# Kernel tuning notes

Measured on AMD Instinct MI355X. Metric: run time of the kernel, lower is better.

The kernel has to match this reference:

```python
import jax, jax.numpy as jnp
import numpy as np

C = 1.0        # curvature parameter (manifold curvature -1/C)
EPS = 1e-7


def expmap0_space(v, k):
    # v: [..., ds] spatial tangent vector at the hyperboloid origin (time comp 0)
    # returns ambient point [..., ds+1] = (sqrt(k)cosh(|v|/sqrt(k)), sqrt(k)sinh(|v|/sqrt(k)) v/|v|)
    sk = jnp.sqrt(k)
    n = jnp.maximum(jnp.linalg.norm(v, axis=-1, keepdims=True), EPS)
    t = sk * jnp.cosh(n / sk)
    s = sk * jnp.sinh(n / sk) * (v / n)
    return jnp.concatenate([t, s], axis=-1)


def logmap0_space(p, k):
    # p: [..., ds+1] hyperboloid point -> spatial tangent [..., ds] at origin
    sk = jnp.sqrt(k)
    t, s = p[..., :1], p[..., 1:]
    ns = jnp.maximum(jnp.linalg.norm(s, axis=-1, keepdims=True), EPS)
    d = sk * jnp.arccosh(jnp.maximum(t / sk, 1.0 + EPS))
    return d * (s / ns)


def setup_inputs() -> dict:
    key = jax.random.key(0)
    N, DS, E = 50000, 127, 800000
    ks = jax.random.split(key, 8)
    x = jax.random.normal(ks[0], (N, DS), dtype=jnp.float32) * 0.1
    edge_src = jax.random.randint(ks[1], (E,), 0, N)
    edge_dst = jax.random.randint(ks[2], (E,), 0, N)
    edge_weight = jax.random.uniform(ks[3], (E,), dtype=jnp.float32) / 16.0  # ~1/deg norm
    sc = 1.0 / np.sqrt(DS)
    W1 = jax.random.normal(ks[4], (DS, DS), dtype=jnp.float32) * sc
    b1 = jnp.zeros((DS,), dtype=jnp.float32)
    W2 = jax.random.normal(ks[5], (DS, DS), dtype=jnp.float32) * sc
    b2 = jnp.zeros((DS,), dtype=jnp.float32)
    return {"x": x, "W1": W1, "b1": b1, "W2": W2, "b2": b2,
            "edge_src": edge_src, "edge_dst": edge_dst, "edge_weight": edge_weight}


def reference(x, W1, b1, W2, b2, edge_src, edge_dst, edge_weight):
    N = x.shape[0]
    # encode(): cat zero time column + expmap0 onto hyperboloid
    p = expmap0_space(x, C)                 # [N, ds+1]
    h = logmap0_space(p, C)                 # tangent features at origin [N, ds]
    for (W, b) in ((W1, b1), (W2, b2)):
        # hyperbolic linear in tangent space
        z = h @ W + b                       # [N, ds]
        # adjacency-based neighbor aggregation (sparse spmm via edge list)
        msg = edge_weight[:, None] * z[edge_src]          # [E, ds] irregular gather
        agg = jax.ops.segment_sum(msg, edge_dst, num_segments=N)
        # activation + skip connection, back onto the manifold between layers
        h = jax.nn.relu(agg) + h
        h = logmap0_space(expmap0_space(h, C), C)
    return expmap0_space(h, C)              # [N, ds+1] on hyperboloid
```

## Files before the change

kernel.cpp:

```cpp
#include <hip/hip_runtime.h>

#define EPS 1e-7f
#define DS 127
#define DP 128
#define NBMAX 512
#define CAP 4096
#define CH 2048
#define PADB ((DP * DP + DP + 255) / 256)
#define BM 64

typedef short bf16x8 __attribute__((ext_vector_type(8)));
typedef float f32x4  __attribute__((ext_vector_type(4)));
typedef float f32x2  __attribute__((ext_vector_type(2)));

__device__ __forceinline__ float wave_sum(float v) {
#pragma unroll
    for (int off = 32; off > 0; off >>= 1)
        v += __shfl_xor(v, off, 64);
    return v;
}

__device__ __forceinline__ int wave_sum_i(int v) {
#pragma unroll
    for (int off = 32; off > 0; off >>= 1)
        v += __shfl_xor(v, off, 64);
    return v;
}

__device__ __forceinline__ unsigned short f2bf(float f) {
    unsigned u = __float_as_uint(f);
    unsigned r = (u + 0x7FFFu + ((u >> 16) & 1u)) >> 16;
    return (unsigned short)r;
}

__device__ __forceinline__ unsigned pack_bf2(float a, float b) {
    return (unsigned)f2bf(a) | ((unsigned)f2bf(b) << 16);
}

__device__ __forceinline__ unsigned char f2fp8(float v) {
    return (unsigned char)(__builtin_amdgcn_cvt_pk_fp8_f32(v, v, 0, false) & 0xFF);
}

__device__ __forceinline__ float logexp_scale(float n2) {
    float nrm = sqrtf(n2);
    return (nrm >= 4.472136e-4f) ? 1.0f : (4.472136e-4f / fmaxf(nrm, EPS));
}

__device__ __forceinline__ void sinhcosh(float n, float& sh, float& ch) {
    float e  = __expf(n);
    float em = __expf(-n);
    sh = 0.5f * (e - em);
    ch = 0.5f * (e + em);
}

__device__ __forceinline__ void padT_dev(int pb, int tid,
        const float* __restrict__ W, const float* __restrict__ b,
        unsigned short* __restrict__ Wt, float* __restrict__ bp) {
    int i = pb * 256 + tid;
    if (i < DP * DP) {
        int n = i >> 7, k = i & (DP - 1);
        Wt[i] = (k < DS && n < DS) ? f2bf(W[k * DS + n]) : (unsigned short)0;
    } else if (i < DP * DP + DP) {
        int j = i - DP * DP;
        bp[j] = (j < DS) ? b[j] : 0.f;
    }
}

__device__ void binA_dev(int abid, int tid,
        const int* __restrict__ es, const int* __restrict__ ed,
        const float* __restrict__ ew,
        int* __restrict__ gcnt, unsigned* __restrict__ stg_pk,
        unsigned char* __restrict__ stg_r, int E) {
    __shared__ int  lcnt[NBMAX];
    __shared__ int  loff[NBMAX];
    __shared__ int  gbase[NBMAX];
    __shared__ unsigned       lst_pk[CH];
    __shared__ unsigned short lst_d[CH];

    int lane = tid & 63;
    int base = abid * CH;
    int cnt  = min(CH, E - base);

    for (int b = tid; b < NBMAX; b += 256) lcnt[b] = 0;
    __syncthreads();

    unsigned pk[CH / 256];
    int      rd[CH / 256];
#pragma unroll
    for (int k = 0; k < CH / 256; k++) {
        int i = base + k * 256 + tid;
        if (i < E) {
            int d = ed[i];
            rd[k] = d;
            pk[k] = ((unsigned)f2bf(ew[i]) << 16) | (unsigned)es[i];
            atomicAdd(&lcnt[d >> 7], 1);
        } else {
            rd[k] = -1;
        }
    }
    __syncthreads();

    if (tid < 64) {
        int carry = 0;
        for (int c = 0; c < NBMAX; c += 64) {
            int v = lcnt[c + lane];
            int inc = v;
#pragma unroll
            for (int off = 1; off < 64; off <<= 1) {
                int t = __shfl_up(inc, off, 64);
                if (lane >= off) inc += t;
            }
            loff[c + lane] = carry + inc - v;
            carry += __shfl(inc, 63, 64);
        }
    }
    __syncthreads();
    for (int b = tid; b < NBMAX; b += 256) lcnt[b] = 0;
    __syncthreads();

#pragma unroll
    for (int k = 0; k < CH / 256; k++) {
        if (rd[k] >= 0) {
            int b = rd[k] >> 7;
            int slot = loff[b] + atomicAdd(&lcnt[b], 1);
            lst_pk[slot] = pk[k];
            lst_d[slot]  = (unsigned short)rd[k];
        }
    }
    __syncthreads();

    for (int b = tid; b < NBMAX; b += 256) {
        int c = lcnt[b];
        gbase[b] = c ? atomicAdd(&gcnt[b], c) : 0;
    }
    __syncthreads();

    for (int s = tid; s < cnt; s += 256) {
        unsigned p = lst_pk[s];
        int d = lst_d[s];
        int b = d >> 7;
        int idx = gbase[b] + (s - loff[b]);
        if (idx >= CAP) idx = CAP - 1;
        stg_pk[(size_t)b * CAP + idx] = p;
        stg_r [(size_t)b * CAP + idx] = (unsigned char)(d & 127);
    }
}

__device__ void binB_dev(int b, int tid,
        const unsigned* __restrict__ stg_pk, const unsigned char* __restrict__ stg_r,
        const int* __restrict__ gcnt,
        int* __restrict__ row_start, unsigned* __restrict__ epk,
        int N, int E) {
    __shared__ int rcnt[128];
    __shared__ int roff[128];
    __shared__ int sh_bb;

    int lane = tid & 63;
    int wave = tid >> 6;
    int cnt  = min(gcnt[b], CAP);
    const unsigned*      in_pk = stg_pk + (size_t)b * CAP;
    const unsigned char* in_r  = stg_r  + (size_t)b * CAP;

    if (tid < 128) rcnt[tid] = 0;
    if (b == 0 && tid == 0) row_start[N] = E;
    __syncthreads();

    if (wave == 3) {
        int acc = 0;
        for (int c = lane; c < b; c += 64) acc += min(gcnt[c], CAP);
        acc = wave_sum_i(acc);
        if (lane == 0) sh_bb = acc;
    } else {
        int n4 = cnt >> 2;
        const uchar4* in_r4 = (const uchar4*)in_r;
        for (int i = tid; i < n4; i += 192) {
            uchar4 v = in_r4[i];
            atomicAdd(&rcnt[v.x], 1);
            atomicAdd(&rcnt[v.y], 1);
            atomicAdd(&rcnt[v.z], 1);
            atomicAdd(&rcnt[v.w], 1);
        }
        for (int i = (n4 << 2) + tid; i < cnt; i += 192)
            atomicAdd(&rcnt[in_r[i]], 1);
    }
    __syncthreads();
    int bb = sh_bb;

    if (tid < 64) {
        int carry = 0;
        for (int c = 0; c < 128; c += 64) {
            int v = rcnt[c + lane];
            int inc = v;
#pragma unroll
            for (int off = 1; off < 64; off <<= 1) {
                int t = __shfl_up(inc, off, 64);
                if (lane >= off) inc += t;
            }
            roff[c + lane] = carry + inc - v;
            carry += __shfl(inc, 63, 64);
        }
    }
    __syncthreads();

    if (tid < 128) {
        int row = b * 128 + tid;
        if (row < N) row_start[row] = bb + roff[tid];
        rcnt[tid] = 0;
    }
    __syncthreads();

    for (int i = tid; i < cnt; i += 256) {
        int r = in_r[i];
        int pos = atomicAdd(&rcnt[r], 1);
        epk[bb + roff[r] + pos] = in_pk[i];
    }
}

__global__ __launch_bounds__(256) void k1_kernel(
        const int* __restrict__ es, const int* __restrict__ ed,
        const float* __restrict__ ew,
        int* __restrict__ gcnt, unsigned* __restrict__ stg_pk,
        unsigned char* __restrict__ stg_r, int E,
        const float* __restrict__ W1, const float* __restrict__ b1,
        unsigned short* __restrict__ Wt1, float* __restrict__ bp1,
        const float* __restrict__ W2, const float* __restrict__ b2,
        unsigned short* __restrict__ Wt2, float* __restrict__ bp2, int nA) {
    int bid = blockIdx.x;
    int tid = threadIdx.x;
    if (bid < nA) {
        binA_dev(bid, tid, es, ed, ew, gcnt, stg_pk, stg_r, E);
        return;
    }
    bid -= nA;
    int layer = (bid >= PADB);
    int pb    = bid - layer * PADB;
    padT_dev(pb, tid, layer ? W2 : W1, layer ? b2 : b1,
             layer ? Wt2 : Wt1, layer ? bp2 : bp1);
}

__device__ void fgemm_dev(int gbid, int tid,
        const float* __restrict__ x, unsigned* __restrict__ hbu,
        const unsigned short* __restrict__ Wt, const float* __restrict__ bp,
        unsigned char* __restrict__ z8, int N) {
    __shared__ unsigned sha[64 * 64];

    int wave = tid >> 6;
    int lane = tid & 63;
    int r0   = gbid * BM;

    f32x2 xv[16];
#pragma unroll
    for (int r = 0; r < 16; r++) {
        int row = r0 + wave * 16 + r;
        if (row < N) {
            const float* rp = x + (size_t)row * DS;
            xv[r].x = rp[2 * lane];
            xv[r].y = (lane < 63) ? rp[2 * lane + 1] : 0.f;
        } else {
            xv[r].x = 0.f; xv[r].y = 0.f;
        }
    }
#pragma unroll
    for (int r = 0; r < 16; r++) {
        int lr  = wave * 16 + r;
        int row = r0 + lr;
        float s = logexp_scale(wave_sum(xv[r].x * xv[r].x + xv[r].y * xv[r].y));
        unsigned pk = pack_bf2(s * xv[r].x, (lane < 63) ? s * xv[r].y : 0.f);
        sha[lr * 64 + lane] = pk;
        if (row < N) hbu[(size_t)row * (DP / 2) + lane] = pk;
    }

    int m    = lane & 15;
    int quad = lane >> 4;

    f32x4 acc[8];
#pragma unroll
    for (int t = 0; t < 8; t++) acc[t] = (f32x4){0.f, 0.f, 0.f, 0.f};

    const unsigned* shrow = sha + (size_t)(wave * 16 + m) * 64;
    bf16x8 a[4];
#pragma unroll
    for (int kq = 0; kq < 4; kq++)
        a[kq] = *(const bf16x8*)(shrow + kq * 16 + quad * 4);

#pragma unroll
    for (int kq = 0; kq < 4; kq++) {
#pragma unroll
        for (int nt = 0; nt < 8; nt++) {
            bf16x8 bfr = ((const bf16x8*)(Wt + (size_t)(nt * 16 + m) * DP))[kq * 4 + quad];
            acc[nt] = __builtin_amdgcn_mfma_f32_16x16x32_bf16(a[kq], bfr, acc[nt], 0, 0, 0);
        }
    }

    int rw0 = r0 + wave * 16;
#pragma unroll
    for (int nt = 0; nt < 8; nt++) {
        float bias = bp[nt * 16 + m];
#pragma unroll
        for (int reg = 0; reg < 4; reg++) {
            int row = rw0 + quad * 4 + reg;
            if (row < N)
                z8[(size_t)row * DP + nt * 16 + m] = f2fp8(acc[nt][reg] + bias);
        }
    }
}

__global__ __launch_bounds__(256) void k2_kernel(
        const unsigned* __restrict__ stg_pk, const unsigned char* __restrict__ stg_r,
        const int* __restrict__ gcnt,
        int* __restrict__ row_start, unsigned* __restrict__ epk,
        const float* __restrict__ x, unsigned* __restrict__ hbu,
        const unsigned short* __restrict__ Wt, const float* __restrict__ bp,
        unsigned char* __restrict__ z8, int N, int E, int nB) {
    int bid = blockIdx.x;
    int tid = threadIdx.x;
    if (bid < nB) {
        binB_dev(bid, tid, stg_pk, stg_r, gcnt, row_start, epk, N, E);
        return;
    }
    fgemm_dev(bid - nB, tid, x, hbu, Wt, bp, z8, N);
}

__global__ __launch_bounds__(256) void gemm_kernel(
        const unsigned short* __restrict__ hb,
        const unsigned short* __restrict__ Wt,
        const float* __restrict__ bp,
        unsigned char* __restrict__ z8, int N) {
    int wave = threadIdx.x >> 6;
    int lane = threadIdx.x & 63;
    int m    = lane & 15;
    int quad = lane >> 4;
    int r0   = blockIdx.x * BM + wave * 16;

    f32x4 acc[8];
#pragma unroll
    for (int t = 0; t < 8; t++) acc[t] = (f32x4){0.f, 0.f, 0.f, 0.f};

    const bf16x8* arow = (const bf16x8*)(hb + (size_t)(r0 + m) * DP);
    bf16x8 a[4];
#pragma unroll
    for (int kq = 0; kq < 4; kq++) a[kq] = arow[kq * 4 + quad];

#pragma unroll
    for (int kq = 0; kq < 4; kq++) {
#pragma unroll
        for (int nt = 0; nt < 8; nt++) {
            bf16x8 bfr = ((const bf16x8*)(Wt + (size_t)(nt * 16 + m) * DP))[kq * 4 + quad];
            acc[nt] = __builtin_amdgcn_mfma_f32_16x16x32_bf16(a[kq], bfr, acc[nt], 0, 0, 0);
        }
    }

#pragma unroll
    for (int nt = 0; nt < 8; nt++) {
        float bias = bp[nt * 16 + m];
#pragma unroll
        for (int reg = 0; reg < 4; reg++) {
            int row = r0 + quad * 4 + reg;
            if (row < N)
                z8[(size_t)row * DP + nt * 16 + m] = f2fp8(acc[nt][reg] + bias);
        }
    }
}

__device__ __forceinline__ void gather16(const unsigned char* __restrict__ zc,
        const unsigned* __restrict__ epk, int e, int lane2,
        float& a0, float& a1) {
    unsigned pks[16], us[16];
#pragma unroll
    for (int i = 0; i < 16; i++) pks[i] = epk[e + i];
#pragma unroll
    for (int i = 0; i < 16; i++)
        us[i] = *(const unsigned short*)(zc + (((pks[i] & 0xFFFFu) << 7) + lane2));
#pragma unroll
    for (int i = 0; i < 16; i++) {
        float wf = __uint_as_float(pks[i] & 0xFFFF0000u);
        f32x2 zv = __builtin_amdgcn_cvt_pk_f32_fp8(us[i], false);
        a0 = fmaf(wf, zv.x, a0);
        a1 = fmaf(wf, zv.y, a1);
    }
}

__device__ __forceinline__ void gather_tail16(const unsigned char* __restrict__ zc,
        const unsigned* __restrict__ epk, int e, int end, int lane2,
        float& a0, float& a1) {
    unsigned pks[16], us[16];
#pragma unroll
    for (int i = 0; i < 16; i++) {
        int ii = e + i;
        int ic = (ii < end) ? ii : (end - 1);
        unsigned p = epk[ic];
        pks[i] = (ii < end) ? p : 0u;
    }
#pragma unroll
    for (int i = 0; i < 16; i++)
        us[i] = *(const unsigned short*)(zc + (((pks[i] & 0xFFFFu) << 7) + lane2));
#pragma unroll
    for (int i = 0; i < 16; i++) {
        float wf = __uint_as_float(pks[i] & 0xFFFF0000u);
        f32x2 zv = __builtin_amdgcn_cvt_pk_f32_fp8(us[i], false);
        a0 = fmaf(wf, zv.x, a0);
        a1 = fmaf(wf, zv.y, a1);
    }
}

template <bool LAST>
__global__ __launch_bounds__(256) void agg_f_tpl(
                          const unsigned char* __restrict__ zc,
                          const unsigned* __restrict__ hbu_in,
                          const int* __restrict__ row_start,
                          const unsigned* __restrict__ epk,
                          unsigned* __restrict__ hbu_out,
                          float* __restrict__ out, int N) {
    int wid  = (int)((blockIdx.x * blockDim.x + threadIdx.x) >> 6);
    int lane = threadIdx.x & 63;
    int gw0  = wid * 2;
    if (gw0 >= N) return;
    gw0 = __builtin_amdgcn_readfirstlane(gw0);
    int lane2 = lane << 1;
    bool has1 = (gw0 + 1 < N);

    int rs0 = row_start[gw0];
    int rs1 = row_start[gw0 + 1];
    int rs2 = has1 ? row_start[gw0 + 2] : rs1;
    unsigned hu0 = hbu_in[(size_t)gw0 * (DP / 2) + lane];
    unsigned hu1 = has1 ? hbu_in[(size_t)(gw0 + 1) * (DP / 2) + lane] : 0u;

    int begs[2] = {rs0, rs1};
    int ends[2] = {rs1, rs2};
    float a0[2] = {0.f, 0.f}, a1[2] = {0.f, 0.f};

#pragma unroll
    for (int r = 0; r < 2; r++) {
        int e = begs[r], end = ends[r];
        for (; e + 16 <= end; e += 16) gather16(zc, epk, e, lane2, a0[r], a1[r]);
        if (e < end) gather_tail16(zc, epk, e, end, lane2, a0[r], a1[r]);
    }

    unsigned hus[2] = {hu0, hu1};
#pragma unroll
    for (int r = 0; r < 2; r++) {
        if (r == 1 && !has1) break;
        int gw = gw0 + r;
        float x0 = __uint_as_float(hus[r] << 16) + fmaxf(a0[r], 0.f);
        float x1 = (lane < 63) ? __uint_as_float(hus[r] & 0xFFFF0000u) + fmaxf(a1[r], 0.f)
                               : 0.f;

        float n2 = wave_sum(x0 * x0 + x1 * x1);
        float scale = logexp_scale(n2);
        float y0 = scale * x0;
        float y1 = (lane < 63) ? scale * x1 : 0.f;

        if (!LAST) {
            hbu_out[(size_t)gw * (DP / 2) + lane] = pack_bf2(y0, y1);
        } else {
            float n2y = scale * scale * n2;
            float ny  = fmaxf(sqrtf(n2y), EPS);
            float shy, chy;
            sinhcosh(ny, shy, chy);
            float sc  = shy / ny;
            float* orow = out + (size_t)gw * DP;
            if (lane == 0) orow[0] = chy;
            orow[1 + 2 * lane] = sc * y0;
            if (lane < 63) orow[2 + 2 * lane] = sc * y1;
        }
    }
}

extern "C" void kernel_launch(void* const* d_in, const int* in_sizes, int n_in,
                              void* d_out, int out_size, void* d_ws, size_t ws_size,
                              hipStream_t stream) {
    const float* x  = (const float*)d_in[0];
    const float* W1 = (const float*)d_in[1];
    const float* b1 = (const float*)d_in[2];
    const float* W2 = (const float*)d_in[3];
    const float* b2 = (const float*)d_in[4];
    const int*   es = (const int*)d_in[5];
    const int*   ed = (const int*)d_in[6];
    const float* ew = (const float*)d_in[7];

    const int N  = in_sizes[0] / DS;
    const int E  = in_sizes[5];
    const int NR = (N + BM - 1) / BM * BM;
    const int NB = (N + 127) >> 7;

    unsigned short* hb  = (unsigned short*)d_ws;
    unsigned char*  z8  = (unsigned char*)(hb + (size_t)NR * DP);
    unsigned short* Wt1 = (unsigned short*)(z8 + (size_t)N * DP);
    unsigned short* Wt2 = Wt1 + DP * DP;
    float* bp1          = (float*)(Wt2 + DP * DP);
    float* bp2          = bp1 + DP;
    unsigned* epk       = (unsigned*)(bp2 + DP);
    int*   row_start    = (int*)(epk + E);
    int*   gcnt         = row_start + N + 1;
    unsigned* stg_pk    = (unsigned*)(gcnt + NBMAX);
    unsigned char* stg_r = (unsigned char*)(stg_pk + (size_t)NBMAX * CAP);

    unsigned* hbu = (unsigned*)hb;

    const int gemmBlocks = (N + BM - 1) / BM;
    const int binABlocks = (E + CH - 1) / CH;
    const int aggWaves   = (N + 1) / 2;
    const int aggBlocks  = (aggWaves + 3) / 4;

    hipMemsetAsync(gcnt, 0, NBMAX * sizeof(int), stream);

    k1_kernel<<<binABlocks + 2 * PADB, 256, 0, stream>>>(
        es, ed, ew, gcnt, stg_pk, stg_r, E,
        W1, b1, Wt1, bp1, W2, b2, Wt2, bp2, binABlocks);

    k2_kernel<<<NB + gemmBlocks, 256, 0, stream>>>(
        stg_pk, stg_r, gcnt, row_start, epk,
        x, hbu, Wt1, bp1, z8, N, E, NB);

    agg_f_tpl<false><<<aggBlocks, 256, 0, stream>>>(z8, hbu, row_start, epk,
                                                    hbu, nullptr, N);

    gemm_kernel<<<gemmBlocks, 256, 0, stream>>>(hb, Wt2, bp2, z8, N);

    agg_f_tpl<true><<<aggBlocks, 256, 0, stream>>>(z8, hbu, row_start, epk,
                                                   nullptr, (float*)d_out, N);
}
```

Baseline: 223.2 us.

## Fuse layer-1 aggregation with layer-2 GEMM via shared-memory staging

Merges the first aggregation kernel and the second-layer GEMM into one kernel. Each block aggregates its 64 rows, stages the bf16 results in LDS and runs the MFMA GEMM from there, writing fp8 z into a new second buffer (z8b) so other blocks' gathers from the old z are not overwritten. This removes a kernel launch and the global round trip of h before the GEMM. The cost is lower parallelism in the aggregation phase, since each wave handles 8 row pairs serially, plus LDS use and an extra N*128-byte workspace buffer.

```diff
diff --git a/kernel.cpp b/kernel.cpp
--- a/kernel.cpp
+++ b/kernel.cpp
@@ -321,47 +321,6 @@
     fgemm_dev(bid - nB, tid, x, hbu, Wt, bp, z8, N);
 }
 
-__global__ __launch_bounds__(256) void gemm_kernel(
-        const unsigned short* __restrict__ hb,
-        const unsigned short* __restrict__ Wt,
-        const float* __restrict__ bp,
-        unsigned char* __restrict__ z8, int N) {
-    int wave = threadIdx.x >> 6;
-    int lane = threadIdx.x & 63;
-    int m    = lane & 15;
-    int quad = lane >> 4;
-    int r0   = blockIdx.x * BM + wave * 16;
-
-    f32x4 acc[8];
-#pragma unroll
-    for (int t = 0; t < 8; t++) acc[t] = (f32x4){0.f, 0.f, 0.f, 0.f};
-
-    const bf16x8* arow = (const bf16x8*)(hb + (size_t)(r0 + m) * DP);
-    bf16x8 a[4];
-#pragma unroll
-    for (int kq = 0; kq < 4; kq++) a[kq] = arow[kq * 4 + quad];
-
-#pragma unroll
-    for (int kq = 0; kq < 4; kq++) {
-#pragma unroll
-        for (int nt = 0; nt < 8; nt++) {
-            bf16x8 bfr = ((const bf16x8*)(Wt + (size_t)(nt * 16 + m) * DP))[kq * 4 + quad];
-            acc[nt] = __builtin_amdgcn_mfma_f32_16x16x32_bf16(a[kq], bfr, acc[nt], 0, 0, 0);
-        }
-    }
-
-#pragma unroll
-    for (int nt = 0; nt < 8; nt++) {
-        float bias = bp[nt * 16 + m];
-#pragma unroll
-        for (int reg = 0; reg < 4; reg++) {
-            int row = r0 + quad * 4 + reg;
-            if (row < N)
-                z8[(size_t)row * DP + nt * 16 + m] = f2fp8(acc[nt][reg] + bias);
-        }
-    }
-}
-
 __device__ __forceinline__ void gather16(const unsigned char* __restrict__ zc,
         const unsigned* __restrict__ epk, int e, int lane2,
         float& a0, float& a1) {
@@ -403,14 +362,112 @@
     }
 }
 
-template <bool LAST>
-__global__ __launch_bounds__(256) void agg_f_tpl(
-                          const unsigned char* __restrict__ zc,
-                          const unsigned* __restrict__ hbu_in,
-                          const int* __restrict__ row_start,
-                          const unsigned* __restrict__ epk,
-                          unsigned* __restrict__ hbu_out,
-                          float* __restrict__ out, int N) {
+__device__ __forceinline__ void agg_pair(const unsigned char* __restrict__ zc,
+        const unsigned* __restrict__ hbu_in,
+        const int* __restrict__ row_start, const unsigned* __restrict__ epk,
+        int gw0, int lane, int lane2, int N,
+        unsigned py[2]) {
+    bool v0 = (gw0 < N);
+    bool v1 = (gw0 + 1 < N);
+    int rs0 = v0 ? row_start[gw0]     : 0;
+    int rs1 = v0 ? row_start[gw0 + 1] : 0;
+    int rs2 = v1 ? row_start[gw0 + 2] : rs1;
+    unsigned hu0 = v0 ? hbu_in[(size_t)gw0 * (DP / 2) + lane]       : 0u;
+    unsigned hu1 = v1 ? hbu_in[(size_t)(gw0 + 1) * (DP / 2) + lane] : 0u;
+
+    int begs[2] = {rs0, rs1};
+    int ends[2] = {rs1, rs2};
+    float a0[2] = {0.f, 0.f}, a1[2] = {0.f, 0.f};
+
+#pragma unroll
+    for (int r = 0; r < 2; r++) {
+        int e = begs[r], end = ends[r];
+        for (; e + 16 <= end; e += 16) gather16(zc, epk, e, lane2, a0[r], a1[r]);
+        if (e < end) gather_tail16(zc, epk, e, end, lane2, a0[r], a1[r]);
+    }
+
+    unsigned hus[2] = {hu0, hu1};
+#pragma unroll
+    for (int r = 0; r < 2; r++) {
+        float x0 = __uint_as_float(hus[r] << 16) + fmaxf(a0[r], 0.f);
+        float x1 = (lane < 63) ? __uint_as_float(hus[r] & 0xFFFF0000u) + fmaxf(a1[r], 0.f)
+                               : 0.f;
+        float n2 = wave_sum(x0 * x0 + x1 * x1);
+        float scale = logexp_scale(n2);
+        py[r] = pack_bf2(scale * x0, (lane < 63) ? scale * x1 : 0.f);
+    }
+}
+
+__global__ __launch_bounds__(256) void k3_kernel(
+        const unsigned char* __restrict__ zc,
+        unsigned* __restrict__ hbu,
+        const int* __restrict__ row_start,
+        const unsigned* __restrict__ epk,
+        const unsigned short* __restrict__ Wt,
+        const float* __restrict__ bp,
+        unsigned char* __restrict__ z8b,
+        int N) {
+    __shared__ unsigned sha[64 * 64];
+
+    int tid = threadIdx.x;
+    int w   = tid >> 6;
+    int ln  = tid & 63;
+    int ln2 = ln << 1;
+    int r0  = blockIdx.x * BM + w * 16;
+
+#pragma unroll 1
+    for (int p = 0; p < 8; p++) {
+        int gw0 = __builtin_amdgcn_readfirstlane(r0 + 2 * p);
+        unsigned py[2];
+        agg_pair(zc, hbu, row_start, epk, gw0, ln, ln2, N, py);
+        int lr = w * 16 + 2 * p;
+        sha[lr * 64 + ln]       = (gw0 < N)     ? py[0] : 0u;
+        sha[(lr + 1) * 64 + ln] = (gw0 + 1 < N) ? py[1] : 0u;
+        if (gw0 < N)     hbu[(size_t)gw0 * (DP / 2) + ln]       = py[0];
+        if (gw0 + 1 < N) hbu[(size_t)(gw0 + 1) * (DP / 2) + ln] = py[1];
+    }
+
+    int m    = ln & 15;
+    int quad = ln >> 4;
+
+    f32x4 acc[8];
+#pragma unroll
+    for (int t = 0; t < 8; t++) acc[t] = (f32x4){0.f, 0.f, 0.f, 0.f};
+
+    const unsigned* shrow = sha + (size_t)(w * 16 + m) * 64;
+    bf16x8 a[4];
+#pragma unroll
+    for (int kq = 0; kq < 4; kq++)
+        a[kq] = *(const bf16x8*)(shrow + kq * 16 + quad * 4);
+
+#pragma unroll
+    for (int kq = 0; kq < 4; kq++) {
+#pragma unroll
+        for (int nt = 0; nt < 8; nt++) {
+            bf16x8 bfr = ((const bf16x8*)(Wt + (size_t)(nt * 16 + m) * DP))[kq * 4 + quad];
+            acc[nt] = __builtin_amdgcn_mfma_f32_16x16x32_bf16(a[kq], bfr, acc[nt], 0, 0, 0);
+        }
+    }
+
+    int rw0 = blockIdx.x * BM + w * 16;
+#pragma unroll
+    for (int nt = 0; nt < 8; nt++) {
+        float bias = bp[nt * 16 + m];
+#pragma unroll
+        for (int reg = 0; reg < 4; reg++) {
+            int row = rw0 + quad * 4 + reg;
+            if (row < N)
+                z8b[(size_t)row * DP + nt * 16 + m] = f2fp8(acc[nt][reg] + bias);
+        }
+    }
+}
+
+__global__ __launch_bounds__(256) void k4_kernel(
+        const unsigned char* __restrict__ zc,
+        const unsigned* __restrict__ hbu_in,
+        const int* __restrict__ row_start,
+        const unsigned* __restrict__ epk,
+        float* __restrict__ out, int N) {
     int wid  = (int)((blockIdx.x * blockDim.x + threadIdx.x) >> 6);
     int lane = threadIdx.x & 63;
     int gw0  = wid * 2;
@@ -450,19 +507,15 @@
         float y0 = scale * x0;
         float y1 = (lane < 63) ? scale * x1 : 0.f;
 
-        if (!LAST) {
-            hbu_out[(size_t)gw * (DP / 2) + lane] = pack_bf2(y0, y1);
-        } else {
-            float n2y = scale * scale * n2;
-            float ny  = fmaxf(sqrtf(n2y), EPS);
-            float shy, chy;
-            sinhcosh(ny, shy, chy);
-            float sc  = shy / ny;
-            float* orow = out + (size_t)gw * DP;
-            if (lane == 0) orow[0] = chy;
-            orow[1 + 2 * lane] = sc * y0;
-            if (lane < 63) orow[2 + 2 * lane] = sc * y1;
-        }
+        float n2y = scale * scale * n2;
+        float ny  = fmaxf(sqrtf(n2y), EPS);
+        float shy, chy;
+        sinhcosh(ny, shy, chy);
+        float sc  = shy / ny;
+        float* orow = out + (size_t)gw * DP;
+        if (lane == 0) orow[0] = chy;
+        orow[1 + 2 * lane] = sc * y0;
+        if (lane < 63) orow[2 + 2 * lane] = sc * y1;
     }
 }
 
@@ -485,7 +538,8 @@
 
     unsigned short* hb  = (unsigned short*)d_ws;
     unsigned char*  z8  = (unsigned char*)(hb + (size_t)NR * DP);
-    unsigned short* Wt1 = (unsigned short*)(z8 + (size_t)N * DP);
+    unsigned char*  z8b = z8 + (size_t)N * DP;
+    unsigned short* Wt1 = (unsigned short*)(z8b + (size_t)N * DP);
     unsigned short* Wt2 = Wt1 + DP * DP;
     float* bp1          = (float*)(Wt2 + DP * DP);
     float* bp2          = bp1 + DP;
@@ -512,11 +566,9 @@
         stg_pk, stg_r, gcnt, row_start, epk,
         x, hbu, Wt1, bp1, z8, N, E, NB);
 
-    agg_f_tpl<false><<<aggBlocks, 256, 0, stream>>>(z8, hbu, row_start, epk,
-                                                    hbu, nullptr, N);
-
-    gemm_kernel<<<gemmBlocks, 256, 0, stream>>>(hb, Wt2, bp2, z8, N);
-
-    agg_f_tpl<true><<<aggBlocks, 256, 0, stream>>>(z8, hbu, row_start, epk,
-                                                   nullptr, (float*)d_out, N);
-}
+    k3_kernel<<<gemmBlocks, 256, 0, stream>>>(
+        z8, hbu, row_start, epk, Wt2, bp2, z8b, N);
+
+    k4_kernel<<<aggBlocks, 256, 0, stream>>>(
+        z8b, hbu, row_start, epk, (float*)d_out, N);
+}
```

Result: no change. 221.9 us (-0.6%).

## Split wave into half-waves gathering alternate edges with 4-byte fp8 loads

Applied to the files above, without the earlier changes.

The aggregation kernel now has each half-wave handle alternating edges. Each lane loads 4 fp8 features per edge as a single 32-bit load instead of 2 bytes, and the two half-wave partial sums are combined with a cross-half shuffle. Both rows' first 32-edge rounds are issued together to expose more independent memory requests. The intent is to halve the number of gather instructions per edge and raise memory-level parallelism. In exchange it reads edge entries past the row end, masked to weight zero, and uses more registers. The histogram loop also drops its uchar4 vectorisation in favour of a plain byte loop.

```diff
diff --git a/kernel.cpp b/kernel.cpp
--- a/kernel.cpp
+++ b/kernel.cpp
@@ -171,16 +171,7 @@
         acc = wave_sum_i(acc);
         if (lane == 0) sh_bb = acc;
     } else {
-        int n4 = cnt >> 2;
-        const uchar4* in_r4 = (const uchar4*)in_r;
-        for (int i = tid; i < n4; i += 192) {
-            uchar4 v = in_r4[i];
-            atomicAdd(&rcnt[v.x], 1);
-            atomicAdd(&rcnt[v.y], 1);
-            atomicAdd(&rcnt[v.z], 1);
-            atomicAdd(&rcnt[v.w], 1);
-        }
-        for (int i = (n4 << 2) + tid; i < cnt; i += 192)
+        for (int i = tid; i < cnt; i += 192)
             atomicAdd(&rcnt[in_r[i]], 1);
     }
     __syncthreads();
@@ -362,44 +353,81 @@
     }
 }
 
-__device__ __forceinline__ void gather16(const unsigned char* __restrict__ zc,
-        const unsigned* __restrict__ epk, int e, int lane2,
-        float& a0, float& a1) {
-    unsigned pks[16], us[16];
-#pragma unroll
-    for (int i = 0; i < 16; i++) pks[i] = epk[e + i];
-#pragma unroll
-    for (int i = 0; i < 16; i++)
-        us[i] = *(const unsigned short*)(zc + (((pks[i] & 0xFFFFu) << 7) + lane2));
+__device__ __forceinline__ void agg_round32(
+        const unsigned char* __restrict__ zc, const unsigned* __restrict__ epk,
+        int e, int end, bool lo, int q4, float* A) {
+    unsigned p[32];
+#pragma unroll
+    for (int i = 0; i < 32; i++) {
+        unsigned v = epk[e + i];
+        p[i] = (e + i < end) ? v : 0u;
+    }
+    unsigned ud[16];
 #pragma unroll
     for (int i = 0; i < 16; i++) {
-        float wf = __uint_as_float(pks[i] & 0xFFFF0000u);
-        f32x2 zv = __builtin_amdgcn_cvt_pk_f32_fp8(us[i], false);
-        a0 = fmaf(wf, zv.x, a0);
-        a1 = fmaf(wf, zv.y, a1);
-    }
-}
-
-__device__ __forceinline__ void gather_tail16(const unsigned char* __restrict__ zc,
-        const unsigned* __restrict__ epk, int e, int end, int lane2,
-        float& a0, float& a1) {
-    unsigned pks[16], us[16];
+        unsigned sel = lo ? p[2 * i] : p[2 * i + 1];
+        ud[i] = *(const unsigned*)(zc + (((size_t)(sel & 0xFFFFu)) << 7) + q4);
+    }
 #pragma unroll
     for (int i = 0; i < 16; i++) {
-        int ii = e + i;
-        int ic = (ii < end) ? ii : (end - 1);
-        unsigned p = epk[ic];
-        pks[i] = (ii < end) ? p : 0u;
-    }
-#pragma unroll
-    for (int i = 0; i < 16; i++)
-        us[i] = *(const unsigned short*)(zc + (((pks[i] & 0xFFFFu) << 7) + lane2));
+        unsigned sel = lo ? p[2 * i] : p[2 * i + 1];
+        float wf = __uint_as_float(sel & 0xFFFF0000u);
+        f32x2 zl = __builtin_amdgcn_cvt_pk_f32_fp8(ud[i], false);
+        f32x2 zh = __builtin_amdgcn_cvt_pk_f32_fp8(ud[i], true);
+        A[0] = fmaf(wf, zl.x, A[0]);
+        A[1] = fmaf(wf, zl.y, A[1]);
+        A[2] = fmaf(wf, zh.x, A[2]);
+        A[3] = fmaf(wf, zh.y, A[3]);
+    }
+}
+
+__device__ __forceinline__ void agg_round32_pair(
+        const unsigned char* __restrict__ zc, const unsigned* __restrict__ epk,
+        int e0, int end0, int e1, int end1, bool lo, int q4,
+        float* A, float* B) {
+    unsigned p0[32], p1[32];
+#pragma unroll
+    for (int i = 0; i < 32; i++) {
+        unsigned v = epk[e0 + i];
+        p0[i] = (e0 + i < end0) ? v : 0u;
+    }
+#pragma unroll
+    for (int i = 0; i < 32; i++) {
+        unsigned v = epk[e1 + i];
+        p1[i] = (e1 + i < end1) ? v : 0u;
+    }
+    unsigned ud0[16], ud1[16];
 #pragma unroll
     for (int i = 0; i < 16; i++) {
-        float wf = __uint_as_float(pks[i] & 0xFFFF0000u);
-        f32x2 zv = __builtin_amdgcn_cvt_pk_f32_fp8(us[i], false);
-        a0 = fmaf(wf, zv.x, a0);
-        a1 = fmaf(wf, zv.y, a1);
+        unsigned sel = lo ? p0[2 * i] : p0[2 * i + 1];
+        ud0[i] = *(const unsigned*)(zc + (((size_t)(sel & 0xFFFFu)) << 7) + q4);
+    }
+#pragma unroll
+    for (int i = 0; i < 16; i++) {
+        unsigned sel = lo ? p1[2 * i] : p1[2 * i + 1];
+        ud1[i] = *(const unsigned*)(zc + (((size_t)(sel & 0xFFFFu)) << 7) + q4);
+    }
+#pragma unroll
+    for (int i = 0; i < 16; i++) {
+        unsigned sel = lo ? p0[2 * i] : p0[2 * i + 1];
+        float wf = __uint_as_float(sel & 0xFFFF0000u);
+        f32x2 zl = __builtin_amdgcn_cvt_pk_f32_fp8(ud0[i], false);
+        f32x2 zh = __builtin_amdgcn_cvt_pk_f32_fp8(ud0[i], true);
+        A[0] = fmaf(wf, zl.x, A[0]);
+        A[1] = fmaf(wf, zl.y, A[1]);
+        A[2] = fmaf(wf, zh.x, A[2]);
+        A[3] = fmaf(wf, zh.y, A[3]);
+    }
+#pragma unroll
+    for (int i = 0; i < 16; i++) {
+        unsigned sel = lo ? p1[2 * i] : p1[2 * i + 1];
+        float wf = __uint_as_float(sel & 0xFFFF0000u);
+        f32x2 zl = __builtin_amdgcn_cvt_pk_f32_fp8(ud1[i], false);
+        f32x2 zh = __builtin_amdgcn_cvt_pk_f32_fp8(ud1[i], true);
+        B[0] = fmaf(wf, zl.x, B[0]);
+        B[1] = fmaf(wf, zl.y, B[1]);
+        B[2] = fmaf(wf, zh.x, B[2]);
+        B[3] = fmaf(wf, zh.y, B[3]);
     }
 }
 
@@ -416,52 +444,71 @@
     int gw0  = wid * 2;
     if (gw0 >= N) return;
     gw0 = __builtin_amdgcn_readfirstlane(gw0);
-    int lane2 = lane << 1;
+    bool lo = (lane < 32);
+    int  q  = lane & 31;
+    int  q4 = q << 2;
     bool has1 = (gw0 + 1 < N);
 
     int rs0 = row_start[gw0];
     int rs1 = row_start[gw0 + 1];
     int rs2 = has1 ? row_start[gw0 + 2] : rs1;
-    unsigned hu0 = hbu_in[(size_t)gw0 * (DP / 2) + lane];
-    unsigned hu1 = has1 ? hbu_in[(size_t)(gw0 + 1) * (DP / 2) + lane] : 0u;
-
-    int begs[2] = {rs0, rs1};
-    int ends[2] = {rs1, rs2};
-    float a0[2] = {0.f, 0.f}, a1[2] = {0.f, 0.f};
-
-#pragma unroll
-    for (int r = 0; r < 2; r++) {
-        int e = begs[r], end = ends[r];
-        for (; e + 16 <= end; e += 16) gather16(zc, epk, e, lane2, a0[r], a1[r]);
-        if (e < end) gather_tail16(zc, epk, e, end, lane2, a0[r], a1[r]);
-    }
-
-    unsigned hus[2] = {hu0, hu1};
+
+    uint2 hu0 = *(const uint2*)(hbu_in + (size_t)gw0 * (DP / 2) + 2 * q);
+    uint2 hu1 = has1 ? *(const uint2*)(hbu_in + (size_t)(gw0 + 1) * (DP / 2) + 2 * q)
+                     : make_uint2(0u, 0u);
+
+    float A[4] = {0.f, 0.f, 0.f, 0.f};
+    float B[4] = {0.f, 0.f, 0.f, 0.f};
+
+    agg_round32_pair(zc, epk, rs0, rs1, rs1, rs2, lo, q4, A, B);
+    int e0 = rs0 + 32, e1 = rs1 + 32;
+    while (e0 < rs1) { agg_round32(zc, epk, e0, rs1, lo, q4, A); e0 += 32; }
+    while (e1 < rs2) { agg_round32(zc, epk, e1, rs2, lo, q4, B); e1 += 32; }
+
+#pragma unroll
+    for (int k = 0; k < 4; k++) {
+        A[k] += __shfl_xor(A[k], 32, 64);
+        B[k] += __shfl_xor(B[k], 32, 64);
+    }
+
+    unsigned hx[2][2] = {{hu0.x, hu0.y}, {hu1.x, hu1.y}};
 #pragma unroll
     for (int r = 0; r < 2; r++) {
         if (r == 1 && !has1) break;
         int gw = gw0 + r;
-        float x0 = __uint_as_float(hus[r] << 16) + fmaxf(a0[r], 0.f);
-        float x1 = (lane < 63) ? __uint_as_float(hus[r] & 0xFFFF0000u) + fmaxf(a1[r], 0.f)
-                               : 0.f;
-
-        float n2 = wave_sum(x0 * x0 + x1 * x1);
+        const float* Ac = (r == 0) ? A : B;
+        float x0 = __uint_as_float(hx[r][0] << 16)          + fmaxf(Ac[0], 0.f);
+        float x1 = __uint_as_float(hx[r][0] & 0xFFFF0000u)  + fmaxf(Ac[1], 0.f);
+        float x2 = __uint_as_float(hx[r][1] << 16)          + fmaxf(Ac[2], 0.f);
+        float x3 = __uint_as_float(hx[r][1] & 0xFFFF0000u)  + fmaxf(Ac[3], 0.f);
+
+        float n2 = x0 * x0 + x1 * x1 + x2 * x2 + x3 * x3;
+#pragma unroll
+        for (int off = 16; off > 0; off >>= 1)
+            n2 += __shfl_xor(n2, off, 64);
+
         float scale = logexp_scale(n2);
-        float y0 = scale * x0;
-        float y1 = (lane < 63) ? scale * x1 : 0.f;
+        float y0 = scale * x0, y1 = scale * x1;
+        float y2 = scale * x2, y3 = scale * x3;
 
         if (!LAST) {
-            hbu_out[(size_t)gw * (DP / 2) + lane] = pack_bf2(y0, y1);
+            unsigned* orow = hbu_out + (size_t)gw * (DP / 2);
+            if (lo) orow[2 * q]     = pack_bf2(y0, y1);
+            else    orow[2 * q + 1] = pack_bf2(y2, y3);
         } else {
-            float n2y = scale * scale * n2;
-            float ny  = fmaxf(sqrtf(n2y), EPS);
+            float ny = fmaxf(scale * sqrtf(n2), EPS);
             float shy, chy;
             sinhcosh(ny, shy, chy);
-            float sc  = shy / ny;
+            float sc = shy / ny;
             float* orow = out + (size_t)gw * DP;
             if (lane == 0) orow[0] = chy;
-            orow[1 + 2 * lane] = sc * y0;
-            if (lane < 63) orow[2 + 2 * lane] = sc * y1;
+            if (lo) {
+                orow[1 + 4 * q] = sc * y0;
+                orow[2 + 4 * q] = sc * y1;
+            } else {
+                orow[3 + 4 * q] = sc * y2;
+                if (q < 31) orow[4 + 4 * q] = sc * y3;
+            }
         }
     }
 }
```

After: 222.1 us. About the same (-0.5%).
